# Optimization experiments

Measured on AMD Instinct MI355X. Metric: run time of the kernel, lower is better.

The kernel has to match this reference:

```python
import jax, jax.numpy as jnp
import numpy as np

N_NODES = 100000
N_EDGES = 3200000
D = 128


def setup_inputs() -> dict:
    key = jax.random.key(0)
    k_feat, k_src, k_dst, k_w1, k_w2 = jax.random.split(key, 5)
    feat = jax.random.normal(k_feat, (N_NODES, D), dtype=jnp.float32)
    src = jax.random.randint(k_src, (N_EDGES,), 0, N_NODES, dtype=jnp.int32)
    dst = jax.random.randint(k_dst, (N_EDGES,), 0, N_NODES, dtype=jnp.int32)
    eps = jnp.zeros((1,), dtype=jnp.float32)
    s1 = 1.0 / np.sqrt(D)
    W1 = jax.random.normal(k_w1, (D, D), dtype=jnp.float32) * s1
    b1 = jnp.zeros((D,), dtype=jnp.float32)
    W2 = jax.random.normal(k_w2, (D, D), dtype=jnp.float32) * s1
    b2 = jnp.zeros((D,), dtype=jnp.float32)
    return {"feat": feat, "src": src, "dst": dst, "eps": eps,
            "W1": W1, "b1": b1, "W2": W2, "b2": b2}


def reference(feat, src, dst, eps, W1, b1, W2, b2):
    # message passing: copy source features along edges, sum-reduce at dst
    # neigh[v] = sum_{(u,v) in E} feat[u]
    msgs = feat[src]                                  # [E, D] gather
    neigh = jax.ops.segment_sum(msgs, dst, num_segments=feat.shape[0])  # [N, D]
    # GIN update: (1 + eps) * h_v + aggregated neighbors, then MLP
    h = (1.0 + eps[0]) * feat + neigh                 # [N, D]
    h = jax.nn.relu(h @ W1 + b1)                      # [N, D]
    out = h @ W2 + b2                                 # [N, D]
    return out
```

## Files before the change

### kernel.cpp

```cpp
#include <hip/hip_runtime.h>
#include <stdint.h>

#define N_NODES 100000
#define N_EDGES 3200000
#define DIM 128
#define NPAD 100032
#define NBINS 391
#define NBLK 782
#define BCAP 10176
#define EPB 4096
#define PASSU32 3200000
#define WSTR 140

typedef short short8 __attribute__((ext_vector_type(8)));
typedef float f32x4 __attribute__((ext_vector_type(4)));
typedef float f32x2 __attribute__((ext_vector_type(2)));

__device__ __forceinline__ short f2bf(float x) {
    uint32_t u = __builtin_bit_cast(uint32_t, x);
    u += 0x7fffu + ((u >> 16) & 1u);
    return (short)(u >> 16);
}
__device__ __forceinline__ float bflo(uint32_t p) {
    return __builtin_bit_cast(float, p << 16);
}
__device__ __forceinline__ float bfhi(uint32_t p) {
    return __builtin_bit_cast(float, p & 0xffff0000u);
}
__device__ __forceinline__ uint32_t pack2(float x, float y) {
    return (uint32_t)(uint16_t)f2bf(x) | ((uint32_t)(uint16_t)f2bf(y) << 16);
}
__device__ __forceinline__ f32x2 up2(uint32_t p) {
    return (f32x2){ bflo(p), bfhi(p) };
}

__global__ __launch_bounds__(256) void prep_kernel(const float* __restrict__ feat,
                                                   uint32_t* __restrict__ featp,
                                                   const float* __restrict__ w1,
                                                   const float* __restrict__ w2,
                                                   short* __restrict__ w1t,
                                                   short* __restrict__ w2t) {
    int b = blockIdx.x, t = threadIdx.x;
    if (b < 12500) {
        int i = b * 256 + t;
        float4 f = ((const float4*)feat)[i];
        int node = i >> 5;
        int qi = i & 31;
        int p = qi >> 4;
        int ld = qi & 15;
        uint32_t* o = &featp[p * PASSU32 + node * 32 + ld * 2];
        o[0] = pack2(f.x, f.y);
        o[1] = pack2(f.z, f.w);
    } else {
        int i = (b - 12500) * 256 + t;
        int k = i >> 7, n = i & 127;
        w1t[n * DIM + k] = f2bf(w1[i]);
        w2t[n * DIM + k] = f2bf(w2[i]);
    }
}

__global__ __launch_bounds__(256) void hist_kernel(const int* __restrict__ dst,
                                                   int* __restrict__ ghist) {
    __shared__ int hist[NBINS];
    int t = threadIdx.x;
    for (int i = t; i < NBINS; i += 256) hist[i] = 0;
    __syncthreads();
    int e0 = blockIdx.x * EPB;
    int nn = min(EPB, N_EDGES - e0);
    for (int i = t; i < nn; i += 256) atomicAdd(&hist[dst[e0 + i] >> 8], 1);
    __syncthreads();
    for (int b = t; b < NBINS; b += 256)
        ghist[b * NBLK + blockIdx.x] = hist[b];
}

__global__ __launch_bounds__(1024) void offset_kernel(const int* __restrict__ ghist,
                                                      int* __restrict__ goff,
                                                      int* __restrict__ bincnt) {
    __shared__ int s[1024];
    int b = blockIdx.x, t = threadIdx.x;
    int v = (t < NBLK) ? ghist[b * NBLK + t] : 0;
    s[t] = v;
    __syncthreads();
    for (int d = 1; d < 1024; d <<= 1) {
        int x = (t >= d) ? s[t - d] : 0;
        __syncthreads();
        s[t] += x;
        __syncthreads();
    }
    if (t < NBLK) goff[b * NBLK + t] = s[t] - v;
    if (t == NBLK - 1) bincnt[b] = s[t];
}

__global__ __launch_bounds__(256) void bin_kernel(const int* __restrict__ src,
                                                  const int* __restrict__ dst,
                                                  const int* __restrict__ goff,
                                                  uint32_t* __restrict__ binpair) {
    __shared__ int hist[512];
    __shared__ int scanv[512];
    __shared__ int scan256[256];
    __shared__ int gbase[NBINS];
    __shared__ int cursor[NBINS];
    __shared__ uint32_t sorted[EPB];
    __shared__ int saddr[EPB];
    int t = threadIdx.x;
    for (int i = t; i < 512; i += 256) hist[i] = 0;
    __syncthreads();
    int e0 = blockIdx.x * EPB;
    int nn = min(EPB, N_EDGES - e0);
    int d[16];
#pragma unroll
    for (int i = 0; i < 16; i++) {
        int idx = i * 256 + t;
        d[i] = (idx < nn) ? dst[e0 + idx] : -1;
        if (d[i] >= 0) atomicAdd(&hist[d[i] >> 8], 1);
    }
    __syncthreads();
    int h0 = hist[2 * t], h1 = hist[2 * t + 1];
    scan256[t] = h0 + h1;
    __syncthreads();
    for (int dd = 1; dd < 256; dd <<= 1) {
        int v = (t >= dd) ? scan256[t - dd] : 0;
        __syncthreads();
        scan256[t] += v;
        __syncthreads();
    }
    int pairExcl = scan256[t] - (h0 + h1);
    scanv[2 * t] = pairExcl;
    scanv[2 * t + 1] = pairExcl + h0;
    for (int b = t; b < NBINS; b += 256) {
        gbase[b] = goff[b * NBLK + blockIdx.x];
        cursor[b] = 0;
    }
    __syncthreads();
#pragma unroll
    for (int i = 0; i < 16; i++) {
        if (d[i] >= 0) {
            int b = d[i] >> 8;
            int slot = atomicAdd(&cursor[b], 1);
            int p = scanv[b] + slot;
            int g = gbase[b] + slot;
            int e = e0 + i * 256 + t;
            sorted[p] = (uint32_t)src[e] | ((uint32_t)(d[i] & 255) << 24);
            saddr[p] = (g < BCAP) ? (b * BCAP + g) : -1;
        }
    }
    __syncthreads();
    for (int i = t; i < nn; i += 256) {
        int a = saddr[i];
        if (a >= 0) binpair[a] = sorted[i];
    }
}

__global__ __launch_bounds__(1024) void csr_kernel(const int* __restrict__ bincnt,
                                                   const uint32_t* __restrict__ binpair,
                                                   int* __restrict__ rowptr,
                                                   int* __restrict__ csr) {
    __shared__ int hist[256];
    __shared__ int cursor[256];
    __shared__ int sc[256];
    __shared__ int red[256];
    __shared__ int binbase_s;
    __shared__ int sorted_s[BCAP];
    int b = blockIdx.x;
    int t = threadIdx.x;
    if (t < 256) {
        int partial = 0;
        for (int j = t; j < b; j += 256) partial += min(bincnt[j], BCAP);
        red[t] = partial;
        hist[t] = 0;
    }
    __syncthreads();
    for (int dd = 128; dd > 0; dd >>= 1) {
        if (t < dd) red[t] += red[t + dd];
        __syncthreads();
    }
    if (t == 0) binbase_s = red[0];
    __syncthreads();
    int binbase = binbase_s;
    int cntb = min(bincnt[b], BCAP);
    const uint32_t* pairs = binpair + (size_t)b * BCAP;
    for (int i = t; i < cntb; i += 1024)
        atomicAdd(&hist[pairs[i] >> 24], 1);
    __syncthreads();
    int val = 0;
    if (t < 256) { val = hist[t]; sc[t] = val; }
    __syncthreads();
    for (int dd = 1; dd < 256; dd <<= 1) {
        int addv = (t < 256 && t >= dd) ? sc[t - dd] : 0;
        __syncthreads();
        if (t < 256) sc[t] += addv;
        __syncthreads();
    }
    if (t < 256) {
        int excl = sc[t] - val;
        rowptr[(b << 8) + t] = binbase + excl;
        cursor[t] = excl;
    }
    __syncthreads();
    for (int i = t; i < cntb; i += 1024) {
        uint32_t p = pairs[i];
        int s2 = atomicAdd(&cursor[p >> 24], 1);
        sorted_s[s2] = (int)(p & 0x00FFFFFFu);
    }
    __syncthreads();
    for (int i = t; i < cntb; i += 1024)
        csr[binbase + i] = sorted_s[i];
}

#define LDQ(qv, sl) do { int _i = __shfl(u, (sl)); \
    qv = *(const uint4*)&featp[_i * 32 + col8 * 4]; } while (0)

#define ACC8(q) do { \
    A01 += up2((q).x); A23 += up2((q).y); A45 += up2((q).z); A67 += up2((q).w); } while (0)

__global__ __launch_bounds__(256) void gather_kernel(const uint32_t* __restrict__ featp,
                                                     const int* __restrict__ rowptr,
                                                     const int* __restrict__ csr,
                                                     const float* __restrict__ eps,
                                                     uint32_t* __restrict__ hbf,
                                                     int poff) {
    int wid = blockIdx.x * 4 + (threadIdx.x >> 6);
    int lane = threadIdx.x & 63;
    int eighth = lane >> 3;
    int col8 = lane & 7;
    if (wid >= N_NODES) {
        if (wid < NPAD && lane < 32) hbf[wid * 64 + poff + lane] = 0;
        return;
    }
    float e1 = 1.0f + eps[0];
    uint4 sf = *(const uint4*)&featp[wid * 32 + col8 * 4];
    f32x2 A01 = (f32x2){0.f, 0.f}, A23 = (f32x2){0.f, 0.f};
    f32x2 A45 = (f32x2){0.f, 0.f}, A67 = (f32x2){0.f, 0.f};
    int start = rowptr[wid], end = rowptr[wid + 1];
    for (int base = start; base < end; base += 64) {
        int m = min(64, end - base);
        int u = (lane < m) ? csr[base + lane] : 0;
        int j = 0;
        for (; j + 32 <= m; j += 32) {
            uint4 q0, q1, q2, q3;
            LDQ(q0, j + eighth);
            LDQ(q1, j + 8 + eighth);
            LDQ(q2, j + 16 + eighth);
            LDQ(q3, j + 24 + eighth);
            ACC8(q0); ACC8(q1); ACC8(q2); ACC8(q3);
        }
        int r = m - j;
        if (r > 0) {
            int mm = m - 1;
            if (r > 24) {
                uint4 q0, q1, q2, q3;
                int p3 = j + 24 + eighth;
                LDQ(q0, j + eighth); LDQ(q1, j + 8 + eighth);
                LDQ(q2, j + 16 + eighth); LDQ(q3, min(p3, mm));
                ACC8(q0); ACC8(q1); ACC8(q2);
                if (p3 < m) ACC8(q3);
            } else if (r > 16) {
                uint4 q0, q1, q2;
                int p2 = j + 16 + eighth;
                LDQ(q0, j + eighth); LDQ(q1, j + 8 + eighth);
                LDQ(q2, min(p2, mm));
                ACC8(q0); ACC8(q1);
                if (p2 < m) ACC8(q2);
            } else if (r > 8) {
                uint4 q0, q1;
                int p1 = j + 8 + eighth;
                LDQ(q0, j + eighth); LDQ(q1, min(p1, mm));
                ACC8(q0);
                if (p1 < m) ACC8(q1);
            } else {
                uint4 q0;
                int p0 = j + eighth;
                LDQ(q0, min(p0, mm));
                if (p0 < m) ACC8(q0);
            }
        }
    }
    float a0 = A01.x, a1 = A01.y, a2 = A23.x, a3 = A23.y;
    float a4 = A45.x, a5 = A45.y, a6 = A67.x, a7 = A67.y;
    a0 += __shfl_xor(a0, 8);  a1 += __shfl_xor(a1, 8);
    a2 += __shfl_xor(a2, 8);  a3 += __shfl_xor(a3, 8);
    a4 += __shfl_xor(a4, 8);  a5 += __shfl_xor(a5, 8);
    a6 += __shfl_xor(a6, 8);  a7 += __shfl_xor(a7, 8);
    a0 += __shfl_xor(a0, 16); a1 += __shfl_xor(a1, 16);
    a2 += __shfl_xor(a2, 16); a3 += __shfl_xor(a3, 16);
    a4 += __shfl_xor(a4, 16); a5 += __shfl_xor(a5, 16);
    a6 += __shfl_xor(a6, 16); a7 += __shfl_xor(a7, 16);
    a0 += __shfl_xor(a0, 32); a1 += __shfl_xor(a1, 32);
    a2 += __shfl_xor(a2, 32); a3 += __shfl_xor(a3, 32);
    a4 += __shfl_xor(a4, 32); a5 += __shfl_xor(a5, 32);
    a6 += __shfl_xor(a6, 32); a7 += __shfl_xor(a7, 32);
    if (eighth == 0) {
        a0 += e1 * bflo(sf.x); a1 += e1 * bfhi(sf.x);
        a2 += e1 * bflo(sf.y); a3 += e1 * bfhi(sf.y);
        a4 += e1 * bflo(sf.z); a5 += e1 * bfhi(sf.z);
        a6 += e1 * bflo(sf.w); a7 += e1 * bfhi(sf.w);
        uint4 w;
        w.x = pack2(a0, a1); w.y = pack2(a2, a3);
        w.z = pack2(a4, a5); w.w = pack2(a6, a7);
        *(uint4*)&hbf[wid * 64 + poff + col8 * 4] = w;
    }
}

__global__ __launch_bounds__(512) void mlp_kernel(const short* __restrict__ hbf,
                                                  const short* __restrict__ w1t,
                                                  const short* __restrict__ w2t,
                                                  const float* __restrict__ b1,
                                                  const float* __restrict__ b2,
                                                  float* __restrict__ out) {
    __shared__ __align__(16) short w1s[128 * WSTR];
    __shared__ __align__(16) short w2s[128 * WSTR];
    __shared__ __align__(16) short h1s[8][16 * WSTR];
    const int t = threadIdx.x;
    for (int c = t; c < 2048; c += 512) {
        int row = c >> 4, cp = c & 15;
        *(short8*)&w1s[row * WSTR + cp * 8] = *(const short8*)&w1t[row * DIM + cp * 8];
        *(short8*)&w2s[row * WSTR + cp * 8] = *(const short8*)&w2t[row * DIM + cp * 8];
    }
    const int wave = t >> 6;
    const int lane = t & 63;
    const int l15 = lane & 15;
    const int quad = lane >> 4;
    short* h1w = &h1s[wave][0];

    float b1v[8], b2v[8];
#pragma unroll
    for (int n = 0; n < 8; n++) {
        b1v[n] = b1[n * 16 + l15];
        b2v[n] = b2[n * 16 + l15];
    }
    __syncthreads();

    const int ngroups = NPAD / 16;
    for (int g = blockIdx.x * 8 + wave; g < ngroups; g += gridDim.x * 8) {
        int row0 = g * 16;
        f32x4 acc[8];
#pragma unroll
        for (int n = 0; n < 8; n++) acc[n] = (f32x4){0.f, 0.f, 0.f, 0.f};
#pragma unroll
        for (int kb = 0; kb < DIM; kb += 32) {
            short8 a = *(const short8*)&hbf[(row0 + l15) * DIM + kb + quad * 8];
#pragma unroll
            for (int n = 0; n < 8; n++) {
                short8 b = *(const short8*)&w1s[(n * 16 + l15) * WSTR + kb + quad * 8];
                acc[n] = __builtin_amdgcn_mfma_f32_16x16x32_bf16(a, b, acc[n], 0, 0, 0);
            }
        }
#pragma unroll
        for (int n = 0; n < 8; n++) {
#pragma unroll
            for (int r = 0; r < 4; r++) {
                float v = acc[n][r] + b1v[n];
                v = v > 0.f ? v : 0.f;
                h1w[(quad * 4 + r) * WSTR + n * 16 + l15] = f2bf(v);
            }
        }
        f32x4 acc2[8];
#pragma unroll
        for (int n = 0; n < 8; n++) acc2[n] = (f32x4){0.f, 0.f, 0.f, 0.f};
#pragma unroll
        for (int kb = 0; kb < DIM; kb += 32) {
            short8 a2 = *(const short8*)&h1w[l15 * WSTR + kb + quad * 8];
#pragma unroll
            for (int n = 0; n < 8; n++) {
                short8 b = *(const short8*)&w2s[(n * 16 + l15) * WSTR + kb + quad * 8];
                acc2[n] = __builtin_amdgcn_mfma_f32_16x16x32_bf16(a2, b, acc2[n], 0, 0, 0);
            }
        }
#pragma unroll
        for (int n = 0; n < 8; n++) {
#pragma unroll
            for (int r = 0; r < 4; r++) {
                int row = row0 + quad * 4 + r;
                if (row < N_NODES)
                    out[row * DIM + n * 16 + l15] = acc2[n][r] + b2v[n];
            }
        }
    }
}

extern "C" void kernel_launch(void* const* d_in, const int* in_sizes, int n_in,
                              void* d_out, int out_size, void* d_ws, size_t ws_size,
                              hipStream_t stream) {
    const float* feat = (const float*)d_in[0];
    const int* src    = (const int*)d_in[1];
    const int* dst    = (const int*)d_in[2];
    const float* eps  = (const float*)d_in[3];
    const float* W1   = (const float*)d_in[4];
    const float* b1   = (const float*)d_in[5];
    const float* W2   = (const float*)d_in[6];
    const float* b2   = (const float*)d_in[7];
    float* out = (float*)d_out;

    char* ws = (char*)d_ws;
    int*      bincnt  = (int*)ws;
    int*      rowptr  = (int*)(ws + 2048);
    int*      csr     = (int*)(ws + 403456);
    uint32_t* binpair = (uint32_t*)(ws + 13203456);
    uint32_t* featp   = (uint32_t*)(ws + 29118720);
    uint32_t* hbf     = (uint32_t*)(ws + 54718720);
    short*    w1t     = (short*)(ws + 80326912);
    short*    w2t     = (short*)(ws + 80359680);
    int*      ghist   = (int*)(ws + 54718720);
    int*      goff    = (int*)(ws + 54718720 + 1223168);

    prep_kernel<<<12564, 256, 0, stream>>>(feat, featp, W1, W2, w1t, w2t);
    hist_kernel<<<NBLK, 256, 0, stream>>>(dst, ghist);
    offset_kernel<<<NBINS, 1024, 0, stream>>>(ghist, goff, bincnt);
    bin_kernel<<<NBLK, 256, 0, stream>>>(src, dst, goff, binpair);
    csr_kernel<<<NBINS, 1024, 0, stream>>>(bincnt, binpair, rowptr, csr);
    gather_kernel<<<NPAD / 4, 256, 0, stream>>>(featp, rowptr, csr, eps, hbf, 0);
    gather_kernel<<<NPAD / 4, 256, 0, stream>>>(featp + PASSU32, rowptr, csr, eps, hbf, 32);
    mlp_kernel<<<256, 512, 0, stream>>>((const short*)hbf, w1t, w2t, b1, b2, out);
}
```

Measured before the change: 305.2 us.

## Split gathered features into eight column slices, one launch with slice-interleaved blocks

The bf16 feature copy is now split into eight 16-column slices (32 bytes per node) instead of two 64-column halves. A single gather launch interleaves the slice index across consecutive blocks, so the blocks running at one time work on the same nodes but touch only a small, cache-resident slice table. Each lane loads 8 bytes per edge in 16-edge groups, and the edge index reads and output stores are now nontemporal. In exchange, the CSR row is read eight times instead of twice, every load is smaller, and there is more shuffle and loop overhead per edge.

```diff
diff --git a/kernel.cpp b/kernel.cpp
--- a/kernel.cpp
+++ b/kernel.cpp
@@ -9,7 +9,7 @@
 #define NBLK 782
 #define BCAP 10176
 #define EPB 4096
-#define PASSU32 3200000
+#define SLU32 800000
 #define WSTR 140
 
 typedef short short8 __attribute__((ext_vector_type(8)));
@@ -46,9 +46,9 @@
         float4 f = ((const float4*)feat)[i];
         int node = i >> 5;
         int qi = i & 31;
-        int p = qi >> 4;
-        int ld = qi & 15;
-        uint32_t* o = &featp[p * PASSU32 + node * 32 + ld * 2];
+        int s = qi >> 2;
+        int w = qi & 3;
+        uint32_t* o = &featp[(size_t)s * SLU32 + node * 8 + w * 2];
         o[0] = pack2(f.x, f.y);
         o[1] = pack2(f.z, f.w);
     } else {
@@ -207,97 +207,60 @@
         csr[binbase + i] = sorted_s[i];
 }
 
-#define LDQ(qv, sl) do { int _i = __shfl(u, (sl)); \
-    qv = *(const uint4*)&featp[_i * 32 + col8 * 4]; } while (0)
-
-#define ACC8(q) do { \
-    A01 += up2((q).x); A23 += up2((q).y); A45 += up2((q).z); A67 += up2((q).w); } while (0)
-
-__global__ __launch_bounds__(256) void gather_kernel(const uint32_t* __restrict__ featp,
+__global__ __launch_bounds__(512) void gather_kernel(const uint32_t* __restrict__ featp,
                                                      const int* __restrict__ rowptr,
                                                      const int* __restrict__ csr,
                                                      const float* __restrict__ eps,
-                                                     uint32_t* __restrict__ hbf,
-                                                     int poff) {
-    int wid = blockIdx.x * 4 + (threadIdx.x >> 6);
+                                                     uint32_t* __restrict__ hbf) {
+    int s = blockIdx.x & 7;
+    int g = blockIdx.x >> 3;
+    int wave = threadIdx.x >> 6;
+    int wid = g * 8 + wave;
     int lane = threadIdx.x & 63;
-    int eighth = lane >> 3;
-    int col8 = lane & 7;
+    int egrp = lane >> 2;
+    int col4 = lane & 3;
+    const uint32_t* fp = featp + (size_t)s * SLU32;
     if (wid >= N_NODES) {
-        if (wid < NPAD && lane < 32) hbf[wid * 64 + poff + lane] = 0;
+        if (wid < NPAD && lane < 8) hbf[wid * 64 + s * 8 + lane] = 0;
         return;
     }
     float e1 = 1.0f + eps[0];
-    uint4 sf = *(const uint4*)&featp[wid * 32 + col8 * 4];
+    uint2 sf = *(const uint2*)&fp[wid * 8 + col4 * 2];
     f32x2 A01 = (f32x2){0.f, 0.f}, A23 = (f32x2){0.f, 0.f};
-    f32x2 A45 = (f32x2){0.f, 0.f}, A67 = (f32x2){0.f, 0.f};
     int start = rowptr[wid], end = rowptr[wid + 1];
     for (int base = start; base < end; base += 64) {
         int m = min(64, end - base);
-        int u = (lane < m) ? csr[base + lane] : 0;
+        int u = 0;
+        if (lane < m) u = __builtin_nontemporal_load(&csr[base + lane]);
         int j = 0;
-        for (; j + 32 <= m; j += 32) {
-            uint4 q0, q1, q2, q3;
-            LDQ(q0, j + eighth);
-            LDQ(q1, j + 8 + eighth);
-            LDQ(q2, j + 16 + eighth);
-            LDQ(q3, j + 24 + eighth);
-            ACC8(q0); ACC8(q1); ACC8(q2); ACC8(q3);
-        }
-        int r = m - j;
-        if (r > 0) {
-            int mm = m - 1;
-            if (r > 24) {
-                uint4 q0, q1, q2, q3;
-                int p3 = j + 24 + eighth;
-                LDQ(q0, j + eighth); LDQ(q1, j + 8 + eighth);
-                LDQ(q2, j + 16 + eighth); LDQ(q3, min(p3, mm));
-                ACC8(q0); ACC8(q1); ACC8(q2);
-                if (p3 < m) ACC8(q3);
-            } else if (r > 16) {
-                uint4 q0, q1, q2;
-                int p2 = j + 16 + eighth;
-                LDQ(q0, j + eighth); LDQ(q1, j + 8 + eighth);
-                LDQ(q2, min(p2, mm));
-                ACC8(q0); ACC8(q1);
-                if (p2 < m) ACC8(q2);
-            } else if (r > 8) {
-                uint4 q0, q1;
-                int p1 = j + 8 + eighth;
-                LDQ(q0, j + eighth); LDQ(q1, min(p1, mm));
-                ACC8(q0);
-                if (p1 < m) ACC8(q1);
-            } else {
-                uint4 q0;
-                int p0 = j + eighth;
-                LDQ(q0, min(p0, mm));
-                if (p0 < m) ACC8(q0);
-            }
+        for (; j + 16 <= m; j += 16) {
+            int idx = __shfl(u, j + egrp);
+            uint2 q = *(const uint2*)&fp[idx * 8 + col4 * 2];
+            A01 += up2(q.x); A23 += up2(q.y);
+        }
+        if (j < m) {
+            int p = j + egrp, mm = m - 1;
+            int idx = __shfl(u, min(p, mm));
+            uint2 q = *(const uint2*)&fp[idx * 8 + col4 * 2];
+            if (p < m) { A01 += up2(q.x); A23 += up2(q.y); }
         }
     }
     float a0 = A01.x, a1 = A01.y, a2 = A23.x, a3 = A23.y;
-    float a4 = A45.x, a5 = A45.y, a6 = A67.x, a7 = A67.y;
+    a0 += __shfl_xor(a0, 4);  a1 += __shfl_xor(a1, 4);
+    a2 += __shfl_xor(a2, 4);  a3 += __shfl_xor(a3, 4);
     a0 += __shfl_xor(a0, 8);  a1 += __shfl_xor(a1, 8);
     a2 += __shfl_xor(a2, 8);  a3 += __shfl_xor(a3, 8);
-    a4 += __shfl_xor(a4, 8);  a5 += __shfl_xor(a5, 8);
-    a6 += __shfl_xor(a6, 8);  a7 += __shfl_xor(a7, 8);
     a0 += __shfl_xor(a0, 16); a1 += __shfl_xor(a1, 16);
     a2 += __shfl_xor(a2, 16); a3 += __shfl_xor(a3, 16);
-    a4 += __shfl_xor(a4, 16); a5 += __shfl_xor(a5, 16);
-    a6 += __shfl_xor(a6, 16); a7 += __shfl_xor(a7, 16);
     a0 += __shfl_xor(a0, 32); a1 += __shfl_xor(a1, 32);
     a2 += __shfl_xor(a2, 32); a3 += __shfl_xor(a3, 32);
-    a4 += __shfl_xor(a4, 32); a5 += __shfl_xor(a5, 32);
-    a6 += __shfl_xor(a6, 32); a7 += __shfl_xor(a7, 32);
-    if (eighth == 0) {
+    if (egrp == 0) {
         a0 += e1 * bflo(sf.x); a1 += e1 * bfhi(sf.x);
         a2 += e1 * bflo(sf.y); a3 += e1 * bfhi(sf.y);
-        a4 += e1 * bflo(sf.z); a5 += e1 * bfhi(sf.z);
-        a6 += e1 * bflo(sf.w); a7 += e1 * bfhi(sf.w);
-        uint4 w;
-        w.x = pack2(a0, a1); w.y = pack2(a2, a3);
-        w.z = pack2(a4, a5); w.w = pack2(a6, a7);
-        *(uint4*)&hbf[wid * 64 + poff + col8 * 4] = w;
+        unsigned long long wv = (unsigned long long)pack2(a0, a1)
+                              | ((unsigned long long)pack2(a2, a3) << 32);
+        __builtin_nontemporal_store(wv,
+            (unsigned long long*)&hbf[wid * 64 + s * 8 + col4 * 2]);
     }
 }
 
@@ -408,7 +371,6 @@
     offset_kernel<<<NBINS, 1024, 0, stream>>>(ghist, goff, bincnt);
     bin_kernel<<<NBLK, 256, 0, stream>>>(src, dst, goff, binpair);
     csr_kernel<<<NBINS, 1024, 0, stream>>>(bincnt, binpair, rowptr, csr);
-    gather_kernel<<<NPAD / 4, 256, 0, stream>>>(featp, rowptr, csr, eps, hbf, 0);
-    gather_kernel<<<NPAD / 4, 256, 0, stream>>>(featp + PASSU32, rowptr, csr, eps, hbf, 32);
+    gather_kernel<<<(NPAD / 8) * 8, 512, 0, stream>>>(featp, rowptr, csr, eps, hbf);
     mlp_kernel<<<256, 512, 0, stream>>>((const short*)hbf, w1t, w2t, b1, b2, out);
 }
```

After: 485.1 us. 59.0% more time.
